# Performance work log

Hardware: AMD Instinct MI355X
Metric: run time of the kernel (lower is better)

## Reference

```python
import jax, jax.numpy as jnp
import numpy as np
from jax import lax

DT = 0.1


def setup_inputs() -> dict:
    key = jax.random.key(0)
    k1, k2, k3, k4 = jax.random.split(key, 4)
    Bsz, L, D, N, O = 32, 2048, 256, 64, 256
    x = jax.random.normal(k1, (Bsz, L, D), dtype=jnp.float32)
    # Shift A by 3*I so Re(eig(A)) > 0 -> bilinear-discretized A_tilde is stable
    A = jax.random.uniform(k2, (N, N), dtype=jnp.float32) + 3.0 * jnp.eye(N, dtype=jnp.float32)
    B = jax.random.uniform(k3, (N, D), dtype=jnp.float32)
    C = jax.random.uniform(k4, (O, N), dtype=jnp.float32)
    return {"x": x, "A": A, "B": B, "C": C}


def _s4_forward(x, A, B, C):
    N = A.shape[0]
    I = jnp.eye(N, dtype=A.dtype)
    # Bilinear discretization (as written in the torch source)
    tmp_inv = jnp.linalg.inv(I + A * (DT / 2))
    A_tilde = tmp_inv @ (I - A * (DT / 2))          # [N, N]
    B_tilde = (tmp_inv @ B) * DT                    # [N, D]

    L = x.shape[1]

    # K[i] = C @ A_tilde^i @ B_tilde; carry M = A_tilde^i @ B_tilde
    def step(M, _):
        return A_tilde @ M, C @ M                    # emit [O, D]

    _, K = lax.scan(step, B_tilde, None, length=L)   # K: [L, O, D]

    n = 2 * L - 1  # length after torch's F.pad(x, (0,0,0,L-1))
    x_fft = jnp.fft.rfft(x, n=n, axis=1)             # [B, F, D] complex
    K_fft = jnp.fft.rfft(K, n=n, axis=0)             # [F, O, D] complex
    y_fft = jnp.einsum('bfi,foi->bfo', x_fft, K_fft)
    y = jnp.fft.irfft(y_fft, n=n, axis=1)[:, :L]     # [B, L, O]
    return y


def reference(x, A, B, C):
    return _s4_forward(x, A, B, C)
```

## Files before the change

### kernel.cpp

```cpp
#include <hip/hip_runtime.h>

#define B_SZ   32
#define LEN    2048
#define DIM    256
#define NST    64
#define OUTD   256
#define CHUNK  64
#define NCHUNK (LEN / CHUNK)
#define ROWS   (B_SZ * LEN)

#define OFF_AT   0
#define OFF_A64  4096
#define OFF_CP   8192
#define OFF_S    24576
#define OFF_INST 90112
#define OFF_V    155648
#define OFF_H    OFF_V
#define WS_FLOATS (OFF_V + (size_t)ROWS * 64)

__device__ __forceinline__ void gload16(const float* gp, float* lds_base,
                                        int lane_off_f) {
#if __has_builtin(__builtin_amdgcn_global_load_lds)
  (void)lane_off_f;
  __builtin_amdgcn_global_load_lds(
      (const __attribute__((address_space(1))) unsigned int*)gp,
      (__attribute__((address_space(3))) unsigned int*)lds_base, 16, 0, 0);
#else
  float4 tmp = *(const float4*)gp;
  *(float4*)(lds_base + lane_off_f) = tmp;
#endif
}

__device__ __forceinline__ void mm64(float* dst, const float* a, const float* b,
                                     int t) {
  const int r0 = 4 * (t >> 4), c0 = 4 * (t & 15);
  float acc[4][4] = {};
  for (int k = 0; k < 64; ++k) {
    float4 bv = *(const float4*)(b + k * 68 + c0);
    for (int i = 0; i < 4; ++i) {
      float av = a[(r0 + i) * 68 + k];
      acc[i][0] = fmaf(av, bv.x, acc[i][0]);
      acc[i][1] = fmaf(av, bv.y, acc[i][1]);
      acc[i][2] = fmaf(av, bv.z, acc[i][2]);
      acc[i][3] = fmaf(av, bv.w, acc[i][3]);
    }
  }
  for (int i = 0; i < 4; ++i)
    *(float4*)(dst + (r0 + i) * 68 + c0) =
        make_float4(acc[i][0], acc[i][1], acc[i][2], acc[i][3]);
  __syncthreads();
}

__global__ __launch_bounds__(256) void k_fused0(const float* __restrict__ A,
                                                const float* __restrict__ Bm,
                                                const float* __restrict__ Cm,
                                                const float* __restrict__ x,
                                                float* __restrict__ ws) {
  __shared__ __align__(16) float sh[13056];
  const int t = threadIdx.x;

  if (blockIdx.x == 0) {
    float* Pa = sh;
    float* Pb = sh + 4352;
    float* Pc = sh + 8704;
    float* rbM = Pc;
    float* rbI = Pc + 128;
    float* cb  = Pc + 256;

    const int tc = t & 63;
    const int tr = t >> 6;
    float M[16], Iv[16];
    for (int i = 0; i < 16; ++i) {
      int r = 16 * tr + i;
      M[i] = 0.05f * A[r * 64 + tc] + (r == tc ? 1.0f : 0.0f);
      Iv[i] = (r == tc) ? 1.0f : 0.0f;
    }
    if (tr == 0) { rbM[tc] = M[0]; rbI[tc] = Iv[0]; }
    if (tc == 0)
      for (int i = 0; i < 16; ++i) cb[16 * tr + i] = M[i];
    __syncthreads();

#pragma unroll
    for (int k = 0; k < 64; ++k) {
      const int cur = (k & 1) * 64, nxt = ((k + 1) & 1) * 64;
      float rinv = 1.0f / rbM[cur + k];
      float rM = rbM[cur + tc] * rinv;
      float rI = rbI[cur + tc] * rinv;
#pragma unroll
      for (int i = 0; i < 16; ++i) {
        int r = 16 * tr + i;
        if (r == k) { M[i] = rM; Iv[i] = rI; }
        else {
          float f = cb[cur + r];
          M[i] = fmaf(-f, rM, M[i]);
          Iv[i] = fmaf(-f, rI, Iv[i]);
        }
      }
      if (k < 63) {
        if (tr == ((k + 1) >> 4)) {
          rbM[nxt + tc] = M[(k + 1) & 15];
          rbI[nxt + tc] = Iv[(k + 1) & 15];
        }
        if (tc == k + 1)
          for (int i = 0; i < 16; ++i) cb[nxt + 16 * tr + i] = M[i];
      }
      __syncthreads();
    }

    for (int i = 0; i < 16; ++i) {
      int r = 16 * tr + i;
      float at = 2.0f * Iv[i] - (r == tc ? 1.0f : 0.0f);
      ws[OFF_AT + r * 64 + tc] = at;
      Pa[r * 68 + tc] = at;
      Pc[r * 68 + tc] = Iv[i];
    }
    __syncthreads();

    mm64(Pb, Pa, Pa, t);
    mm64(Pa, Pb, Pb, t);
    mm64(Pb, Pa, Pa, t);
    mm64(Pa, Pb, Pb, t);
    mm64(Pb, Pa, Pa, t);
    mm64(Pa, Pb, Pb, t);
    for (int i = 0; i < 16; ++i) {
      int r = 16 * tr + i;
      ws[OFF_A64 + r * 64 + tc] = Pa[r * 68 + tc];
    }

    {
      const float* Crow = Cm + (size_t)t * 64;
      float4 acc4[16];
      for (int q = 0; q < 16; ++q) acc4[q] = make_float4(0.f, 0.f, 0.f, 0.f);
      for (int k = 0; k < 64; k += 4) {
        float4 c4 = *(const float4*)(Crow + k);
        float ck[4] = {c4.x, c4.y, c4.z, c4.w};
#pragma unroll
        for (int kk = 0; kk < 4; ++kk) {
          const float* mrow = Pc + (k + kk) * 68;
          float c = ck[kk];
#pragma unroll
          for (int q = 0; q < 16; ++q) {
            float4 mv = *(const float4*)(mrow + 4 * q);
            acc4[q].x = fmaf(c, mv.x, acc4[q].x);
            acc4[q].y = fmaf(c, mv.y, acc4[q].y);
            acc4[q].z = fmaf(c, mv.z, acc4[q].z);
            acc4[q].w = fmaf(c, mv.w, acc4[q].w);
          }
        }
      }
      float* cp = ws + OFF_CP + (size_t)t * 64;
      for (int q = 0; q < 16; ++q)
        *(float4*)(cp + 4 * q) =
            make_float4(0.1f * acc4[q].x, 0.1f * acc4[q].y, 0.1f * acc4[q].z,
                        0.1f * acc4[q].w);
    }
  } else {
    float* xs0 = sh;
    float* xs1 = sh + 4096;
    float* bs0 = sh + 8192;
    float* bs1 = sh + 10240;
    const int w = t >> 6, lane = t & 63;
    const int ro8 = lane >> 3, kq8 = lane & 7;
    const int rowbase = ((int)blockIdx.x - 1) * 128;

    auto stage = [&](int d0, float* xbuf, float* bbuf) {
#pragma unroll
      for (int c = 0; c < 4; ++c) {
        int q = 4 * w + c;
        const float* gp = x + (size_t)(rowbase + 8 * q + ro8) * 256 + d0 +
                          4 * (kq8 ^ (q & 7));
        gload16(gp, xbuf + q * 256, lane * 4);
      }
#pragma unroll
      for (int c = 0; c < 2; ++c) {
        int q = 2 * w + c;
        const float* gp =
            Bm + (size_t)(8 * q + ro8) * 256 + d0 + 4 * (kq8 ^ q);
        gload16(gp, bbuf + q * 256, lane * 4);
      }
    };

    stage(0, xs0, bs0);
    const int g = lane >> 4, lm = lane & 15;
    const int r0 = 32 * w + 8 * g, m0 = 4 * lm;
    const int ka = 4 * ((4 * w + g) & 7);
    const int kb = 4 * ((lm >> 1) & 7);
    float acc[8][4] = {};
    float* xc = xs0; float* xn = xs1; float* bc = bs0; float* bn = bs1;
    __syncthreads();

    for (int s = 0; s < 8; ++s) {
      if (s < 7) stage((s + 1) * 32, xn, bn);
      const float* xa = xc + r0 * 32;
      const float* bb = bc + m0 * 32;
#pragma unroll
      for (int k0 = 0; k0 < 32; k0 += 4) {
        float4 a4[8], b4[4];
#pragma unroll
        for (int i = 0; i < 8; ++i)
          a4[i] = *(const float4*)(xa + i * 32 + (k0 ^ ka));
#pragma unroll
        for (int j = 0; j < 4; ++j)
          b4[j] = *(const float4*)(bb + j * 32 + (k0 ^ kb));
#pragma unroll
        for (int i = 0; i < 8; ++i)
#pragma unroll
          for (int j = 0; j < 4; ++j) {
            acc[i][j] = fmaf(a4[i].x, b4[j].x, acc[i][j]);
            acc[i][j] = fmaf(a4[i].y, b4[j].y, acc[i][j]);
            acc[i][j] = fmaf(a4[i].z, b4[j].z, acc[i][j]);
            acc[i][j] = fmaf(a4[i].w, b4[j].w, acc[i][j]);
          }
      }
      __syncthreads();
      float* tp;
      tp = xc; xc = xn; xn = tp;
      tp = bc; bc = bn; bn = tp;
    }
    float* v = ws + OFF_V;
#pragma unroll
    for (int i = 0; i < 8; ++i)
      *(float4*)(v + (size_t)(rowbase + r0 + i) * 64 + m0) =
          make_float4(acc[i][0], acc[i][1], acc[i][2], acc[i][3]);
  }
}

__device__ __forceinline__ void load_areg(const float* __restrict__ M, int r,
                                          int q, float areg[16]) {
  const float4* ap = (const float4*)(M + r * 64 + q * 16);
  float4 a0 = ap[0], a1 = ap[1], a2 = ap[2], a3 = ap[3];
  areg[0] = a0.x; areg[1] = a0.y; areg[2] = a0.z; areg[3] = a0.w;
  areg[4] = a1.x; areg[5] = a1.y; areg[6] = a1.z; areg[7] = a1.w;
  areg[8] = a2.x; areg[9] = a2.y; areg[10] = a2.z; areg[11] = a2.w;
  areg[12] = a3.x; areg[13] = a3.y; areg[14] = a3.z; areg[15] = a3.w;
}

__device__ __forceinline__ float matvec_step(const float areg[16],
                                             const float* __restrict__ hcur,
                                             float* __restrict__ part, int r,
                                             int q, int t) {
  float4 ha = *(const float4*)(hcur + q * 16);
  float4 hb = *(const float4*)(hcur + q * 16 + 4);
  float4 hc = *(const float4*)(hcur + q * 16 + 8);
  float4 hd = *(const float4*)(hcur + q * 16 + 12);
  float p0 = fmaf(areg[0], ha.x, fmaf(areg[4], hb.x, fmaf(areg[8], hc.x, areg[12] * hd.x)));
  float p1 = fmaf(areg[1], ha.y, fmaf(areg[5], hb.y, fmaf(areg[9], hc.y, areg[13] * hd.y)));
  float p2 = fmaf(areg[2], ha.z, fmaf(areg[6], hb.z, fmaf(areg[10], hc.z, areg[14] * hd.z)));
  float p3 = fmaf(areg[3], ha.w, fmaf(areg[7], hb.w, fmaf(areg[11], hc.w, areg[15] * hd.w)));
  part[q * 68 + r] = (p0 + p1) + (p2 + p3);
  __syncthreads();
  float s = 0.0f;
  if (t < 64) s = part[t] + part[68 + t] + part[136 + t] + part[204 + t];
  return s;
}

__global__ __launch_bounds__(256) void k_chunk(float* __restrict__ ws, int phase) {
  __shared__ __align__(16) float hcur[64];
  __shared__ __align__(16) float part[4 * 68];
  __shared__ __align__(16) float ulds[CHUNK * 64];
  const int t = threadIdx.x;
  const int c = blockIdx.x, b = blockIdx.y;
  const int r = t & 63, q = t >> 6;
  float areg[16];
  load_areg(ws + OFF_AT, r, q, areg);
  const float* u = ws + OFF_V + (size_t)(b * LEN + c * CHUNK) * 64;
  for (int i = 0; i < 4; ++i) {
    int e = 4 * (t + 256 * i);
    *(float4*)(ulds + e) = *(const float4*)(u + e);
  }
  if (t < 64)
    hcur[t] = (phase == 3) ? ws[OFF_INST + (b * NCHUNK + c) * 64 + t] : 0.0f;
  __syncthreads();
  for (int st = 0; st < CHUNK; ++st) {
    float s = matvec_step(areg, hcur, part, r, q, t);
    if (t < 64) {
      float hn = s + ulds[st * 64 + t];
      hcur[t] = hn;
      if (phase == 3)
        ws[OFF_H + (size_t)(b * LEN + c * CHUNK + st) * 64 + t] = hn;
      else if (st == CHUNK - 1)
        ws[OFF_S + (b * NCHUNK + c) * 64 + t] = hn;
    }
    __syncthreads();
  }
}

__global__ __launch_bounds__(256) void k_carry(float* __restrict__ ws) {
  __shared__ __align__(16) float hcur[64];
  __shared__ __align__(16) float part[4 * 68];
  __shared__ __align__(16) float slds[NCHUNK * 64];
  const int t = threadIdx.x;
  const int b = blockIdx.x;
  const int r = t & 63, q = t >> 6;
  float areg[16];
  load_areg(ws + OFF_A64, r, q, areg);
  for (int i = 0; i < 2; ++i) {
    int e = 4 * (t + 256 * i);
    *(float4*)(slds + e) = *(const float4*)(ws + OFF_S + b * NCHUNK * 64 + e);
  }
  if (t < 64) {
    hcur[t] = 0.0f;
    ws[OFF_INST + (b * NCHUNK) * 64 + t] = 0.0f;
  }
  __syncthreads();
  for (int c = 1; c < NCHUNK; ++c) {
    float s = matvec_step(areg, hcur, part, r, q, t);
    if (t < 64) {
      float hn = s + slds[(c - 1) * 64 + t];
      hcur[t] = hn;
      ws[OFF_INST + (b * NCHUNK + c) * 64 + t] = hn;
    }
    __syncthreads();
  }
}

__global__ __launch_bounds__(256) void k_ygemm(const float* __restrict__ ws,
                                               float* __restrict__ y) {
  __shared__ __align__(16) float sh[16384];
  float* hs = sh;
  float* cs = sh + 8192;
  const int t = threadIdx.x;
  const int w = t >> 6, lane = t & 63;
  const int rowbase = blockIdx.x * 128;
  const int obase = blockIdx.y * 128;
  const float* H = ws + OFF_H;
  const float* CP = ws + OFF_CP;

  const int ro4 = lane >> 4, kq16 = lane & 15;
#pragma unroll
  for (int c = 0; c < 8; ++c) {
    int q = 8 * w + c;
    int row = 4 * q + ro4;
    int sd = 4 * (kq16 ^ ((row >> 3) & 7));
    gload16(H + (size_t)(rowbase + row) * 64 + sd, hs + q * 256, lane * 4);
    gload16(CP + (size_t)(obase + row) * 64 + sd, cs + q * 256, lane * 4);
  }
  __syncthreads();

  const int g = lane >> 4, lm = lane & 15;
  const int r0 = 32 * w + 8 * g, o0 = 8 * lm;
  const int ka = 4 * ((4 * w + g) & 7);
  const int kb = 4 * (lm & 7);
  const float* ha = hs + r0 * 64;
  const float* cbp = cs + o0 * 64;
  float acc[8][8] = {};
#pragma unroll
  for (int k0 = 0; k0 < 64; k0 += 4) {
    float4 a4[8], b4[8];
#pragma unroll
    for (int i = 0; i < 8; ++i)
      a4[i] = *(const float4*)(ha + i * 64 + (k0 ^ ka));
#pragma unroll
    for (int j = 0; j < 8; ++j)
      b4[j] = *(const float4*)(cbp + j * 64 + (k0 ^ kb));
#pragma unroll
    for (int i = 0; i < 8; ++i)
#pragma unroll
      for (int j = 0; j < 8; ++j) {
        acc[i][j] = fmaf(a4[i].x, b4[j].x, acc[i][j]);
        acc[i][j] = fmaf(a4[i].y, b4[j].y, acc[i][j]);
        acc[i][j] = fmaf(a4[i].z, b4[j].z, acc[i][j]);
        acc[i][j] = fmaf(a4[i].w, b4[j].w, acc[i][j]);
      }
  }
#pragma unroll
  for (int i = 0; i < 8; ++i) {
    float* yp = y + (size_t)(rowbase + r0 + i) * 256 + obase + o0;
    *(float4*)(yp) = make_float4(acc[i][0], acc[i][1], acc[i][2], acc[i][3]);
    *(float4*)(yp + 4) = make_float4(acc[i][4], acc[i][5], acc[i][6], acc[i][7]);
  }
}

extern "C" void kernel_launch(void* const* d_in, const int* in_sizes, int n_in,
                              void* d_out, int out_size, void* d_ws,
                              size_t ws_size, hipStream_t stream) {
  const float* x = (const float*)d_in[0];
  const float* A = (const float*)d_in[1];
  const float* Bm = (const float*)d_in[2];
  const float* Cm = (const float*)d_in[3];
  float* y = (float*)d_out;
  float* ws = (float*)d_ws;
  if (ws_size < (size_t)WS_FLOATS * sizeof(float)) return;

  hipLaunchKernelGGL(k_fused0, dim3(1 + ROWS / 128), dim3(256), 0, stream, A,
                     Bm, Cm, x, ws);
  hipLaunchKernelGGL(k_chunk, dim3(NCHUNK, B_SZ), dim3(256), 0, stream, ws, 1);
  hipLaunchKernelGGL(k_carry, dim3(B_SZ), dim3(256), 0, stream, ws);
  hipLaunchKernelGGL(k_chunk, dim3(NCHUNK, B_SZ), dim3(256), 0, stream, ws, 3);
  hipLaunchKernelGGL(k_ygemm, dim3(ROWS / 128, OUTD / 128), dim3(256), 0,
                     stream, ws, y);
}
```

Measured before the change: 260.3 us.

## Fuse output GEMM into chunk scan, two-step recurrence, larger V tiles

Removes the separate y GEMM kernel and computes y = H·C' per chunk inside the phase-3 chunk kernel from LDS-resident states, so the full H array is no longer written to and read back from global memory. The intra-chunk recurrence now advances two timesteps per serial iteration using a precomputed A^2, with the A·u terms computed in parallel beforehand, which halves the number of barrier-separated sequential steps. The C·Minv precompute moves to an extra block of the first chunk launch, and the x·B^T GEMM tile grows to 256 rows with an 8x8 register tile. The trade-offs are more registers and LDS per block, a small GEMM done with lower parallelism per block, and an extra block that adds to the phase-1 launch.

```diff
diff --git a/kernel.cpp b/kernel.cpp
--- a/kernel.cpp
+++ b/kernel.cpp
@@ -10,12 +10,13 @@
 #define ROWS   (B_SZ * LEN)
 
 #define OFF_AT   0
-#define OFF_A64  4096
-#define OFF_CP   8192
-#define OFF_S    24576
-#define OFF_INST 90112
-#define OFF_V    155648
-#define OFF_H    OFF_V
+#define OFF_P2   4096
+#define OFF_P64  8192
+#define OFF_MINV 12288
+#define OFF_CP   16384
+#define OFF_S    32768
+#define OFF_INST 98304
+#define OFF_V    163840
 #define WS_FLOATS (OFF_V + (size_t)ROWS * 64)
 
 __device__ __forceinline__ void gload16(const float* gp, float* lds_base,
@@ -37,6 +38,7 @@
   float acc[4][4] = {};
   for (int k = 0; k < 64; ++k) {
     float4 bv = *(const float4*)(b + k * 68 + c0);
+#pragma unroll
     for (int i = 0; i < 4; ++i) {
       float av = a[(r0 + i) * 68 + k];
       acc[i][0] = fmaf(av, bv.x, acc[i][0]);
@@ -45,31 +47,31 @@
       acc[i][3] = fmaf(av, bv.w, acc[i][3]);
     }
   }
+#pragma unroll
   for (int i = 0; i < 4; ++i)
     *(float4*)(dst + (r0 + i) * 68 + c0) =
         make_float4(acc[i][0], acc[i][1], acc[i][2], acc[i][3]);
   __syncthreads();
 }
 
-__global__ __launch_bounds__(256) void k_fused0(const float* __restrict__ A,
-                                                const float* __restrict__ Bm,
-                                                const float* __restrict__ Cm,
-                                                const float* __restrict__ x,
-                                                float* __restrict__ ws) {
-  __shared__ __align__(16) float sh[13056];
+__global__ __launch_bounds__(256, 1) void k_fused0(const float* __restrict__ A,
+                                                   const float* __restrict__ Bm,
+                                                   const float* __restrict__ x,
+                                                   float* __restrict__ ws) {
+  __shared__ __align__(16) float sh[20480];
   const int t = threadIdx.x;
 
   if (blockIdx.x == 0) {
-    float* Pa = sh;
-    float* Pb = sh + 4352;
-    float* Pc = sh + 8704;
-    float* rbM = Pc;
-    float* rbI = Pc + 128;
-    float* cb  = Pc + 256;
+    float* Pa  = sh;
+    float* Pb  = sh + 4352;
+    float* rbM = sh + 8704;
+    float* rbI = sh + 8832;
+    float* cb  = sh + 8960;
 
     const int tc = t & 63;
     const int tr = t >> 6;
     float M[16], Iv[16];
+#pragma unroll
     for (int i = 0; i < 16; ++i) {
       int r = 16 * tr + i;
       M[i] = 0.05f * A[r * 64 + tc] + (r == tc ? 1.0f : 0.0f);
@@ -107,66 +109,45 @@
       __syncthreads();
     }
 
+#pragma unroll
     for (int i = 0; i < 16; ++i) {
       int r = 16 * tr + i;
       float at = 2.0f * Iv[i] - (r == tc ? 1.0f : 0.0f);
       ws[OFF_AT + r * 64 + tc] = at;
+      ws[OFF_MINV + r * 64 + tc] = Iv[i];
       Pa[r * 68 + tc] = at;
-      Pc[r * 68 + tc] = Iv[i];
     }
     __syncthreads();
 
     mm64(Pb, Pa, Pa, t);
+#pragma unroll
+    for (int i = 0; i < 16; ++i) {
+      int r = 16 * tr + i;
+      ws[OFF_P2 + r * 64 + tc] = Pb[r * 68 + tc];
+    }
     mm64(Pa, Pb, Pb, t);
     mm64(Pb, Pa, Pa, t);
     mm64(Pa, Pb, Pb, t);
     mm64(Pb, Pa, Pa, t);
     mm64(Pa, Pb, Pb, t);
+#pragma unroll
     for (int i = 0; i < 16; ++i) {
       int r = 16 * tr + i;
-      ws[OFF_A64 + r * 64 + tc] = Pa[r * 68 + tc];
-    }
-
-    {
-      const float* Crow = Cm + (size_t)t * 64;
-      float4 acc4[16];
-      for (int q = 0; q < 16; ++q) acc4[q] = make_float4(0.f, 0.f, 0.f, 0.f);
-      for (int k = 0; k < 64; k += 4) {
-        float4 c4 = *(const float4*)(Crow + k);
-        float ck[4] = {c4.x, c4.y, c4.z, c4.w};
-#pragma unroll
-        for (int kk = 0; kk < 4; ++kk) {
-          const float* mrow = Pc + (k + kk) * 68;
-          float c = ck[kk];
-#pragma unroll
-          for (int q = 0; q < 16; ++q) {
-            float4 mv = *(const float4*)(mrow + 4 * q);
-            acc4[q].x = fmaf(c, mv.x, acc4[q].x);
-            acc4[q].y = fmaf(c, mv.y, acc4[q].y);
-            acc4[q].z = fmaf(c, mv.z, acc4[q].z);
-            acc4[q].w = fmaf(c, mv.w, acc4[q].w);
-          }
-        }
-      }
-      float* cp = ws + OFF_CP + (size_t)t * 64;
-      for (int q = 0; q < 16; ++q)
-        *(float4*)(cp + 4 * q) =
-            make_float4(0.1f * acc4[q].x, 0.1f * acc4[q].y, 0.1f * acc4[q].z,
-                        0.1f * acc4[q].w);
+      ws[OFF_P64 + r * 64 + tc] = Pa[r * 68 + tc];
     }
   } else {
     float* xs0 = sh;
-    float* xs1 = sh + 4096;
-    float* bs0 = sh + 8192;
-    float* bs1 = sh + 10240;
+    float* xs1 = sh + 8192;
+    float* bs0 = sh + 16384;
+    float* bs1 = sh + 18432;
     const int w = t >> 6, lane = t & 63;
     const int ro8 = lane >> 3, kq8 = lane & 7;
-    const int rowbase = ((int)blockIdx.x - 1) * 128;
+    const int rowbase = ((int)blockIdx.x - 1) * 256;
 
     auto stage = [&](int d0, float* xbuf, float* bbuf) {
 #pragma unroll
-      for (int c = 0; c < 4; ++c) {
-        int q = 4 * w + c;
+      for (int c = 0; c < 8; ++c) {
+        int q = 8 * w + c;
         const float* gp = x + (size_t)(rowbase + 8 * q + ro8) * 256 + d0 +
                           4 * (kq8 ^ (q & 7));
         gload16(gp, xbuf + q * 256, lane * 4);
@@ -181,11 +162,12 @@
     };
 
     stage(0, xs0, bs0);
-    const int g = lane >> 4, lm = lane & 15;
-    const int r0 = 32 * w + 8 * g, m0 = 4 * lm;
-    const int ka = 4 * ((4 * w + g) & 7);
-    const int kb = 4 * ((lm >> 1) & 7);
-    float acc[8][4] = {};
+    const int rg = lane >> 3, mg = lane & 7;
+    const int r0 = 64 * w + 8 * rg;
+    const int m0 = 8 * mg;
+    const int ka = 4 * rg;
+    const int kb = 4 * mg;
+    float acc[8][8] = {};
     float* xc = xs0; float* xn = xs1; float* bc = bs0; float* bn = bs1;
     __syncthreads();
 
@@ -195,17 +177,17 @@
       const float* bb = bc + m0 * 32;
 #pragma unroll
       for (int k0 = 0; k0 < 32; k0 += 4) {
-        float4 a4[8], b4[4];
+        float4 a4[8], b4[8];
 #pragma unroll
         for (int i = 0; i < 8; ++i)
           a4[i] = *(const float4*)(xa + i * 32 + (k0 ^ ka));
 #pragma unroll
-        for (int j = 0; j < 4; ++j)
+        for (int j = 0; j < 8; ++j)
           b4[j] = *(const float4*)(bb + j * 32 + (k0 ^ kb));
 #pragma unroll
         for (int i = 0; i < 8; ++i)
 #pragma unroll
-          for (int j = 0; j < 4; ++j) {
+          for (int j = 0; j < 8; ++j) {
             acc[i][j] = fmaf(a4[i].x, b4[j].x, acc[i][j]);
             acc[i][j] = fmaf(a4[i].y, b4[j].y, acc[i][j]);
             acc[i][j] = fmaf(a4[i].z, b4[j].z, acc[i][j]);
@@ -219,9 +201,12 @@
     }
     float* v = ws + OFF_V;
 #pragma unroll
-    for (int i = 0; i < 8; ++i)
-      *(float4*)(v + (size_t)(rowbase + r0 + i) * 64 + m0) =
-          make_float4(acc[i][0], acc[i][1], acc[i][2], acc[i][3]);
+    for (int i = 0; i < 8; ++i) {
+      float* vp = v + (size_t)(rowbase + r0 + i) * 64 + m0;
+      *(float4*)(vp) = make_float4(acc[i][0], acc[i][1], acc[i][2], acc[i][3]);
+      *(float4*)(vp + 4) =
+          make_float4(acc[i][4], acc[i][5], acc[i][6], acc[i][7]);
+    }
   }
 }
 
@@ -254,34 +239,207 @@
   return s;
 }
 
-__global__ __launch_bounds__(256) void k_chunk(float* __restrict__ ws, int phase) {
-  __shared__ __align__(16) float hcur[64];
-  __shared__ __align__(16) float part[4 * 68];
-  __shared__ __align__(16) float ulds[CHUNK * 64];
+__global__ __launch_bounds__(256) void k_chunk(float* __restrict__ ws,
+                                               const float* __restrict__ Cm,
+                                               float* __restrict__ y,
+                                               int phase) {
+  __shared__ __align__(16) float sh[11360];
+  float* ulds  = sh;
+  float* wbuf  = sh + 4352;
+  float* wpart = sh + 6400;
+  float* partb = sh + 10752;
+  float* hcur  = sh + 11296;
   const int t = threadIdx.x;
+
+  if (blockIdx.x == NCHUNK) {
+    if (blockIdx.y != 0) return;
+    float* Ms = sh;
+    float* Cs = wpart;
+#pragma unroll
+    for (int i = 0; i < 4; ++i) {
+      int e = 4 * (t + 256 * i);
+      int kk = e >> 6, nn = e & 63;
+      *(float4*)(Ms + kk * 68 + nn) = *(const float4*)(ws + OFF_MINV + e);
+    }
+    __syncthreads();
+    const int r0 = 4 * (t >> 4), c0 = 4 * (t & 15);
+    for (int ob = 0; ob < 4; ++ob) {
+#pragma unroll
+      for (int i = 0; i < 4; ++i) {
+        int e = 4 * (t + 256 * i);
+        int orow = e >> 6, kk = e & 63;
+        *(float4*)(Cs + orow * 68 + kk) =
+            *(const float4*)(Cm + (size_t)(64 * ob + orow) * 64 + kk);
+      }
+      __syncthreads();
+      float acc[4][4] = {};
+      for (int k = 0; k < 64; ++k) {
+        float4 bv = *(const float4*)(Ms + k * 68 + c0);
+#pragma unroll
+        for (int i = 0; i < 4; ++i) {
+          float av = Cs[(r0 + i) * 68 + k];
+          acc[i][0] = fmaf(av, bv.x, acc[i][0]);
+          acc[i][1] = fmaf(av, bv.y, acc[i][1]);
+          acc[i][2] = fmaf(av, bv.z, acc[i][2]);
+          acc[i][3] = fmaf(av, bv.w, acc[i][3]);
+        }
+      }
+#pragma unroll
+      for (int i = 0; i < 4; ++i)
+        *(float4*)(ws + OFF_CP + (size_t)(64 * ob + r0 + i) * 64 + c0) =
+            make_float4(0.1f * acc[i][0], 0.1f * acc[i][1], 0.1f * acc[i][2],
+                        0.1f * acc[i][3]);
+      __syncthreads();
+    }
+    return;
+  }
+
   const int c = blockIdx.x, b = blockIdx.y;
   const int r = t & 63, q = t >> 6;
-  float areg[16];
+  float areg[16], areg2[16];
   load_areg(ws + OFF_AT, r, q, areg);
+  load_areg(ws + OFF_P2, r, q, areg2);
+
   const float* u = ws + OFF_V + (size_t)(b * LEN + c * CHUNK) * 64;
+#pragma unroll
   for (int i = 0; i < 4; ++i) {
     int e = 4 * (t + 256 * i);
-    *(float4*)(ulds + e) = *(const float4*)(u + e);
+    int row = e >> 6, col = e & 63;
+    *(float4*)(ulds + row * 68 + (col ^ (row & 28))) =
+        *(const float4*)(u + e);
   }
   if (t < 64)
     hcur[t] = (phase == 3) ? ws[OFF_INST + (b * NCHUNK + c) * 64 + t] : 0.0f;
   __syncthreads();
-  for (int st = 0; st < CHUNK; ++st) {
-    float s = matvec_step(areg, hcur, part, r, q, t);
+
+  for (int sw = 0; sw < 2; ++sw) {
+#pragma unroll
+    for (int jj = 0; jj < 16; ++jj) {
+      int j = 16 * sw + jj;
+      int rowe = 2 * j;
+      int s2 = rowe & 28;
+      const float* ub = ulds + rowe * 68;
+      float p = 0.0f;
+#pragma unroll
+      for (int cq = 0; cq < 4; ++cq) {
+        float4 uv = *(const float4*)(ub + ((16 * q + 4 * cq) ^ s2));
+        p = fmaf(areg[4 * cq + 0], uv.x, p);
+        p = fmaf(areg[4 * cq + 1], uv.y, p);
+        p = fmaf(areg[4 * cq + 2], uv.z, p);
+        p = fmaf(areg[4 * cq + 3], uv.w, p);
+      }
+      wpart[jj * 272 + q * 68 + r] = p;
+    }
+    __syncthreads();
+    {
+      int jj = t >> 4;
+      int j = 16 * sw + jj;
+      int m4 = 4 * (t & 15);
+      int rowo = 2 * j + 1;
+      int s2o = rowo & 28;
+      float4 s = make_float4(0.f, 0.f, 0.f, 0.f);
+#pragma unroll
+      for (int qq = 0; qq < 4; ++qq) {
+        float4 pv = *(const float4*)(wpart + jj * 272 + qq * 68 + m4);
+        s.x += pv.x; s.y += pv.y; s.z += pv.z; s.w += pv.w;
+      }
+      float4 uo = *(const float4*)(ulds + rowo * 68 + (m4 ^ s2o));
+      s.x += uo.x; s.y += uo.y; s.z += uo.z; s.w += uo.w;
+      *(float4*)(wbuf + j * 64 + m4) = s;
+    }
+    __syncthreads();
+  }
+
+  float* part1 = partb;
+  float* part2 = partb + 272;
+  for (int j = 0; j < 32; ++j) {
+    float4 h0 = *(const float4*)(hcur + 16 * q);
+    float4 h1 = *(const float4*)(hcur + 16 * q + 4);
+    float4 h2 = *(const float4*)(hcur + 16 * q + 8);
+    float4 h3 = *(const float4*)(hcur + 16 * q + 12);
+    float p2v;
+    {
+      float a0 = fmaf(areg2[0], h0.x, fmaf(areg2[4], h1.x,
+                 fmaf(areg2[8], h2.x, areg2[12] * h3.x)));
+      float a1 = fmaf(areg2[1], h0.y, fmaf(areg2[5], h1.y,
+                 fmaf(areg2[9], h2.y, areg2[13] * h3.y)));
+      float a2 = fmaf(areg2[2], h0.z, fmaf(areg2[6], h1.z,
+                 fmaf(areg2[10], h2.z, areg2[14] * h3.z)));
+      float a3 = fmaf(areg2[3], h0.w, fmaf(areg2[7], h1.w,
+                 fmaf(areg2[11], h2.w, areg2[15] * h3.w)));
+      p2v = (a0 + a1) + (a2 + a3);
+    }
+    part2[q * 68 + r] = p2v;
+    if (phase == 3) {
+      float a0 = fmaf(areg[0], h0.x, fmaf(areg[4], h1.x,
+                 fmaf(areg[8], h2.x, areg[12] * h3.x)));
+      float a1 = fmaf(areg[1], h0.y, fmaf(areg[5], h1.y,
+                 fmaf(areg[9], h2.y, areg[13] * h3.y)));
+      float a2 = fmaf(areg[2], h0.z, fmaf(areg[6], h1.z,
+                 fmaf(areg[10], h2.z, areg[14] * h3.z)));
+      float a3 = fmaf(areg[3], h0.w, fmaf(areg[7], h1.w,
+                 fmaf(areg[11], h2.w, areg[15] * h3.w)));
+      part1[q * 68 + r] = (a0 + a1) + (a2 + a3);
+    }
+    __syncthreads();
     if (t < 64) {
-      float hn = s + ulds[st * 64 + t];
-      hcur[t] = hn;
-      if (phase == 3)
-        ws[OFF_H + (size_t)(b * LEN + c * CHUNK + st) * 64 + t] = hn;
-      else if (st == CHUNK - 1)
-        ws[OFF_S + (b * NCHUNK + c) * 64 + t] = hn;
-    }
-    __syncthreads();
+      float s2 = part2[t] + part2[68 + t] + part2[136 + t] + part2[204 + t];
+      int rowe = 2 * j, rowo = 2 * j + 1;
+      float ho = s2 + wbuf[j * 64 + t];
+      if (phase == 3) {
+        float s1 = part1[t] + part1[68 + t] + part1[136 + t] + part1[204 + t];
+        float he = s1 + ulds[rowe * 68 + (t ^ (rowe & 28))];
+        ulds[rowe * 68 + (t ^ (rowe & 28))] = he;
+        ulds[rowo * 68 + (t ^ (rowo & 28))] = ho;
+      } else if (j == 31) {
+        ws[OFF_S + (b * NCHUNK + c) * 64 + t] = ho;
+      }
+      hcur[t] = ho;
+    }
+    __syncthreads();
+  }
+
+  if (phase == 3) {
+    float* cps = wpart;
+    const int r0e = 4 * (t >> 4), o0 = 4 * (t & 15);
+    for (int p = 0; p < 4; ++p) {
+#pragma unroll
+      for (int i = 0; i < 4; ++i) {
+        int e = 4 * (t + 256 * i);
+        int orow = e >> 6, nn = e & 63;
+        *(float4*)(cps + orow * 68 + (nn ^ (orow & 28))) =
+            *(const float4*)(ws + OFF_CP + (size_t)(64 * p + orow) * 64 + nn);
+      }
+      __syncthreads();
+      float acc[4][4] = {};
+#pragma unroll
+      for (int n0 = 0; n0 < 64; n0 += 4) {
+        float4 a4[4], b4[4];
+#pragma unroll
+        for (int i = 0; i < 4; ++i)
+          a4[i] = *(const float4*)(ulds + (r0e + i) * 68 +
+                                   (n0 ^ ((r0e + i) & 28)));
+#pragma unroll
+        for (int jj = 0; jj < 4; ++jj)
+          b4[jj] = *(const float4*)(cps + (o0 + jj) * 68 +
+                                    (n0 ^ ((o0 + jj) & 28)));
+#pragma unroll
+        for (int i = 0; i < 4; ++i)
+#pragma unroll
+          for (int jj = 0; jj < 4; ++jj) {
+            acc[i][jj] = fmaf(a4[i].x, b4[jj].x, acc[i][jj]);
+            acc[i][jj] = fmaf(a4[i].y, b4[jj].y, acc[i][jj]);
+            acc[i][jj] = fmaf(a4[i].z, b4[jj].z, acc[i][jj]);
+            acc[i][jj] = fmaf(a4[i].w, b4[jj].w, acc[i][jj]);
+          }
+      }
+#pragma unroll
+      for (int i = 0; i < 4; ++i)
+        *(float4*)(y + (size_t)(b * LEN + c * CHUNK + r0e + i) * 256 +
+                   64 * p + o0) =
+            make_float4(acc[i][0], acc[i][1], acc[i][2], acc[i][3]);
+      __syncthreads();
+    }
   }
 }
 
@@ -293,7 +451,7 @@
   const int b = blockIdx.x;
   const int r = t & 63, q = t >> 6;
   float areg[16];
-  load_areg(ws + OFF_A64, r, q, areg);
+  load_areg(ws + OFF_P64, r, q, areg);
   for (int i = 0; i < 2; ++i) {
     int e = 4 * (t + 256 * i);
     *(float4*)(slds + e) = *(const float4*)(ws + OFF_S + b * NCHUNK * 64 + e);
@@ -311,63 +469,6 @@
       ws[OFF_INST + (b * NCHUNK + c) * 64 + t] = hn;
     }
     __syncthreads();
-  }
-}
-
-__global__ __launch_bounds__(256) void k_ygemm(const float* __restrict__ ws,
-                                               float* __restrict__ y) {
-  __shared__ __align__(16) float sh[16384];
-  float* hs = sh;
-  float* cs = sh + 8192;
-  const int t = threadIdx.x;
-  const int w = t >> 6, lane = t & 63;
-  const int rowbase = blockIdx.x * 128;
-  const int obase = blockIdx.y * 128;
-  const float* H = ws + OFF_H;
-  const float* CP = ws + OFF_CP;
-
-  const int ro4 = lane >> 4, kq16 = lane & 15;
-#pragma unroll
-  for (int c = 0; c < 8; ++c) {
-    int q = 8 * w + c;
-    int row = 4 * q + ro4;
-    int sd = 4 * (kq16 ^ ((row >> 3) & 7));
-    gload16(H + (size_t)(rowbase + row) * 64 + sd, hs + q * 256, lane * 4);
-    gload16(CP + (size_t)(obase + row) * 64 + sd, cs + q * 256, lane * 4);
-  }
-  __syncthreads();
-
-  const int g = lane >> 4, lm = lane & 15;
-  const int r0 = 32 * w + 8 * g, o0 = 8 * lm;
-  const int ka = 4 * ((4 * w + g) & 7);
-  const int kb = 4 * (lm & 7);
-  const float* ha = hs + r0 * 64;
-  const float* cbp = cs + o0 * 64;
-  float acc[8][8] = {};
-#pragma unroll
-  for (int k0 = 0; k0 < 64; k0 += 4) {
-    float4 a4[8], b4[8];
-#pragma unroll
-    for (int i = 0; i < 8; ++i)
-      a4[i] = *(const float4*)(ha + i * 64 + (k0 ^ ka));
-#pragma unroll
-    for (int j = 0; j < 8; ++j)
-      b4[j] = *(const float4*)(cbp + j * 64 + (k0 ^ kb));
-#pragma unroll
-    for (int i = 0; i < 8; ++i)
-#pragma unroll
-      for (int j = 0; j < 8; ++j) {
-        acc[i][j] = fmaf(a4[i].x, b4[j].x, acc[i][j]);
-        acc[i][j] = fmaf(a4[i].y, b4[j].y, acc[i][j]);
-        acc[i][j] = fmaf(a4[i].z, b4[j].z, acc[i][j]);
-        acc[i][j] = fmaf(a4[i].w, b4[j].w, acc[i][j]);
-      }
-  }
-#pragma unroll
-  for (int i = 0; i < 8; ++i) {
-    float* yp = y + (size_t)(rowbase + r0 + i) * 256 + obase + o0;
-    *(float4*)(yp) = make_float4(acc[i][0], acc[i][1], acc[i][2], acc[i][3]);
-    *(float4*)(yp + 4) = make_float4(acc[i][4], acc[i][5], acc[i][6], acc[i][7]);
   }
 }
 
@@ -382,11 +483,11 @@
   float* ws = (float*)d_ws;
   if (ws_size < (size_t)WS_FLOATS * sizeof(float)) return;
 
-  hipLaunchKernelGGL(k_fused0, dim3(1 + ROWS / 128), dim3(256), 0, stream, A,
-                     Bm, Cm, x, ws);
-  hipLaunchKernelGGL(k_chunk, dim3(NCHUNK, B_SZ), dim3(256), 0, stream, ws, 1);
+  hipLaunchKernelGGL(k_fused0, dim3(1 + ROWS / 256), dim3(256), 0, stream, A,
+                     Bm, x, ws);
+  hipLaunchKernelGGL(k_chunk, dim3(NCHUNK + 1, B_SZ), dim3(256), 0, stream, ws,
+                     Cm, y, 1);
   hipLaunchKernelGGL(k_carry, dim3(B_SZ), dim3(256), 0, stream, ws);
-  hipLaunchKernelGGL(k_chunk, dim3(NCHUNK, B_SZ), dim3(256), 0, stream, ws, 3);
-  hipLaunchKernelGGL(k_ygemm, dim3(ROWS / 128, OUTD / 128), dim3(256), 0,
-                     stream, ws, y);
-}
+  hipLaunchKernelGGL(k_chunk, dim3(NCHUNK, B_SZ), dim3(256), 0, stream, ws, Cm,
+                     y, 3);
+}
```

After: 275.8 us. 1.06x slower.
